# Kernel tuning notes

Measured on AMD Instinct MI355X. Metric: run time of the kernel, lower is better.

The kernel has to match this reference:

```python
import jax, jax.numpy as jnp
import numpy as np

N = 40000            # atoms
ER = 2_500_000       # radial edges
EA = 1_200_000       # angular edges
P = 4_000_000        # angle triples
NUM_SPECIES = 4      # H,C,N,O
CUTOFF = 5.2
ANG_CUTOFF = 3.5
RADIAL_ETA = 16.0
ANGULAR_ETA = 8.0
RDIV = 16
ADIV = 4
ZETA = 32.0
ASEC = 4
RSTART = 0.8
ASTART = 0.8


def setup_inputs() -> dict:
    key = jax.random.key(0)
    ks = jax.random.split(key, 12)
    species = jax.random.randint(ks[0], (N,), 0, NUM_SPECIES, dtype=jnp.int32)
    rad_distances = jax.random.uniform(ks[1], (ER,), jnp.float32, RSTART, CUTOFF)
    rad_switch = jax.random.uniform(ks[2], (ER,), jnp.float32)
    edge_src = jax.random.randint(ks[3], (ER,), 0, N, dtype=jnp.int32)
    edge_dst = jax.random.randint(ks[4], (ER,), 0, N, dtype=jnp.int32)
    ang_distances = jax.random.uniform(ks[5], (EA,), jnp.float32, ASTART, ANG_CUTOFF)
    ang_switch = jax.random.uniform(ks[6], (EA,), jnp.float32)
    angles = jax.random.uniform(ks[7], (P,), jnp.float32, 0.0, float(np.pi))
    central_atom = jax.random.randint(ks[8], (P,), 0, N, dtype=jnp.int32)
    angle_src = jax.random.randint(ks[9], (P,), 0, EA, dtype=jnp.int32)
    angle_dst = jax.random.randint(ks[10], (P,), 0, EA, dtype=jnp.int32)
    ang_edge_dst = jax.random.randint(ks[11], (EA,), 0, N, dtype=jnp.int32)
    return {
        "species": species,
        "rad_distances": rad_distances,
        "rad_switch": rad_switch,
        "edge_src": edge_src,
        "edge_dst": edge_dst,
        "ang_distances": ang_distances,
        "ang_switch": ang_switch,
        "angles": angles,
        "central_atom": central_atom,
        "angle_src": angle_src,
        "angle_dst": angle_dst,
        "ang_edge_dst": ang_edge_dst,
    }


def _triu_table(nsp):
    s1, s2 = np.triu_indices(nsp, 0)
    t = np.zeros((nsp, nsp), dtype=np.int32)
    t[s1, s2] = np.arange(s1.shape[0], dtype=np.int32)
    t[s2, s1] = t[s1, s2]
    return jnp.asarray(t)


def reference(species, rad_distances, rad_switch, edge_src, edge_dst,
              ang_distances, ang_switch, angles, central_atom,
              angle_src, angle_dst, ang_edge_dst):
    n_atoms = species.shape[0]
    nsp = NUM_SPECIES
    nsp_pair = nsp * (nsp + 1) // 2
    indices = species  # already species-order indices in [0, nsp)

    # ---- radial AEV ----
    shiftR = jnp.asarray(-np.linspace(RSTART, CUTOFF, RDIV + 1)[None, :-1],
                         dtype=rad_distances.dtype)  # [1, RDIV]
    x2 = RADIAL_ETA * (rad_distances[:, None] + shiftR) ** 2       # [ER, RDIV]
    radial_terms = jnp.exp(-x2) * (0.25 * rad_switch)[:, None]
    radial_index = edge_src * nsp + indices[edge_dst]
    radial_aev = jax.ops.segment_sum(radial_terms, radial_index,
                                     num_segments=nsp * n_atoms)
    radial_aev = radial_aev.reshape(n_atoms, nsp * RDIV)

    # ---- angular AEV ----
    dist = 0.5 * ANGULAR_ETA ** 0.5 * ang_distances                # [EA]
    d12 = (dist[angle_src] + dist[angle_dst])[:, None]             # [P, 1]
    angle_start = np.pi / (2 * ASEC)
    shiftZ = jnp.asarray(-(np.linspace(0, np.pi, ASEC + 1) + angle_start)[None, :-1],
                         dtype=dist.dtype)                          # [1, ASEC]
    shiftA = jnp.asarray(-ANGULAR_ETA ** 0.5 *
                         np.linspace(ASTART, ANG_CUTOFF, ADIV + 1)[None, :-1],
                         dtype=dist.dtype)                          # [1, ADIV]
    sw = ang_switch * (2.0 * 0.5 ** ZETA) ** 0.5                   # [EA]
    f1 = sw[angle_src] * sw[angle_dst]                             # [P]
    factor1 = f1[:, None] * (1 + jnp.cos(angles[:, None] + shiftZ)) ** ZETA  # [P, ASEC]
    factor2 = jnp.exp(-(d12 + shiftA) ** 2)                        # [P, ADIV]
    angular_terms = (factor1[:, None, :] * factor2[:, :, None]).reshape(-1, ASEC * ADIV)

    idx_dest = indices[ang_edge_dst]                               # [EA]
    triu = _triu_table(nsp)
    angular_index = central_atom * nsp_pair + triu[idx_dest[angle_src], idx_dest[angle_dst]]
    angular_aev = jax.ops.segment_sum(angular_terms, angular_index,
                                      num_segments=nsp_pair * n_atoms)
    angular_aev = angular_aev.reshape(n_atoms, nsp_pair * ASEC * ADIV)

    return jnp.concatenate((radial_aev, angular_aev), axis=-1)     # [N, 224]
```

## Files before the change

### kernel.cpp

```cpp
#include <hip/hip_runtime.h>


constexpr int kOutCols  = 224;
constexpr int kAngBase  = 64;
constexpr int kABUCK    = 64;
constexpr int kMaxBins  = 640;
constexpr int kSCap     = 4096;
constexpr int kNBR      = 640;
constexpr int kNBA      = 1024;
constexpr int kRCap     = 4608;
constexpr int kACap     = 7168;
constexpr int kRC       = 12;
constexpr int kCapR     = 16;
constexpr int kCapA     = 12;
constexpr int kOvf      = 512;

__device__ __constant__ int c_triu[16] = {0,1,2,3, 1,4,5,6, 2,5,7,8, 3,6,8,9};
__device__ __constant__ float c_ca[4] = {0.92387953f, 0.38268343f, -0.38268343f, -0.92387953f};
__device__ __constant__ float c_sa[4] = {0.38268343f, 0.92387953f,  0.92387953f,  0.38268343f};
__device__ __constant__ float c_sh[4] = {-2.2627417f, -4.1719303f, -6.0811183f, -7.9903066f};

constexpr float kThQ  = 20860.437f;
constexpr float kRevD = 7.6295109e-6f;
constexpr float kD12B = 2.2627417f;
constexpr float kD12S = 1.4974026e-2f;
constexpr float kF1D  = 1.1732081e-13f;
constexpr float kRdS  = 930.6818f;
constexpr float kRdD  = 1.0744811e-3f;
constexpr float kRswD = 6.1050061e-5f;

__device__ __forceinline__ int scan1024_exc(int cv, int tid, int* wsum, int* total)
{
    int lane = tid & 63, wv = tid >> 6;
    int x = cv;
    #pragma unroll
    for (int o = 1; o < 64; o <<= 1) {
        int t = __shfl_up(x, o, 64);
        if (lane >= o) x += t;
    }
    if (lane == 63) wsum[wv] = x;
    __syncthreads();
    if (wv == 0 && lane < 16) {
        int s = wsum[lane];
        #pragma unroll
        for (int o = 1; o < 16; o <<= 1) {
            int t = __shfl_up(s, o, 64);
            if (lane >= o) s += t;
        }
        wsum[lane] = s;
    }
    __syncthreads();
    int base = (wv == 0) ? 0 : wsum[wv - 1];
    *total = wsum[15];
    return base + x - cv;
}

__global__ __launch_bounds__(1024)
void fused1(const float* __restrict__ rd, const float* __restrict__ rsw,
            const int* __restrict__ esrc, const int* __restrict__ edst,
            const int* __restrict__ species,
            unsigned* __restrict__ rrec, int* __restrict__ offRT, int ER, int chR,
            const float* __restrict__ ang_d, const float* __restrict__ ang_sw,
            const int* __restrict__ aed, unsigned short* __restrict__ eaq, int EA)
{
    __shared__ unsigned stage[kMaxBins * kCapR];
    __shared__ int cur[kMaxBins], off[kMaxBins + 1];
    __shared__ int wsum[16];
    __shared__ int ovfn;
    __shared__ uint4 ovfb[kOvf];
    int tid = threadIdx.x;

    if (blockIdx.x < kNBR) {
        for (int t = tid; t < kMaxBins; t += 1024) cur[t] = t * kCapR;
        if (tid == 0) ovfn = 0;
        __syncthreads();
        int sb  = blockIdx.x;
        int beg = sb * chR, end = min(beg + chR, ER);
        int i0 = beg + tid * 4;
        if (i0 < end) {
            float4 d4 = *reinterpret_cast<const float4*>(rd + i0);
            float4 s4 = *reinterpret_cast<const float4*>(rsw + i0);
            int4   e4 = *reinterpret_cast<const int4*>(esrc + i0);
            int4   t4 = *reinterpret_cast<const int4*>(edst + i0);
            unsigned sa = (unsigned)species[t4.x], sb2 = (unsigned)species[t4.y];
            unsigned sc2 = (unsigned)species[t4.z], sd = (unsigned)species[t4.w];
            auto bld = [](float d, float s, int e, unsigned sp, unsigned& v, int& k) {
                unsigned qd = min((unsigned)(fmaxf(d - 0.8f, 0.0f) * kRdS + 0.5f), 4095u);
                unsigned qs = min((unsigned)(fmaxf(s, 0.0f) * 4095.0f + 0.5f), 4095u);
                v = qd | (qs << 12) | (sp << 24) | ((unsigned)(e & 63) << 26);
                k = e >> 6;
            };
            unsigned v0, v1, v2, v3; int k0, k1, k2, k3;
            bld(d4.x, s4.x, e4.x, sa,  v0, k0);
            bld(d4.y, s4.y, e4.y, sb2, v1, k1);
            bld(d4.z, s4.z, e4.z, sc2, v2, k2);
            bld(d4.w, s4.w, e4.w, sd,  v3, k3);
            auto ins = [&](int k, unsigned v) {
                int pos = atomicAdd(&cur[k], 1);
                int loc = pos - k * kCapR;
                if (loc < kCapR) stage[pos] = v;
                else {
                    int o = atomicAdd(&ovfn, 1);
                    if (o < kOvf) { ovfb[o].x = (unsigned)k; ovfb[o].y = (unsigned)loc; ovfb[o].z = v; }
                }
            };
            ins(k0, v0); ins(k1, v1); ins(k2, v2); ins(k3, v3);
        }
        __syncthreads();
        int cv = (tid < kMaxBins) ? (cur[tid] - tid * kCapR) : 0;
        int tot;
        int exc = scan1024_exc(cv, tid, wsum, &tot);
        if (tid < kMaxBins) off[tid] = exc;
        if (tid == 0) off[kMaxBins] = tot;
        if (tid < kMaxBins) cur[tid] = min(cv, kCapR);
        __syncthreads();
        for (int s = tid; s < kMaxBins * kCapR; s += 1024) {
            int bin = s >> 4, loc = s & (kCapR - 1);
            if (loc < cur[bin]) rrec[beg + off[bin] + loc] = stage[s];
        }
        int no = min(ovfn, kOvf);
        for (int o = tid; o < no; o += 1024) {
            uint4 e = ovfb[o];
            rrec[beg + off[e.x] + (int)e.y] = e.z;
        }
        for (int t = tid; t <= kMaxBins; t += 1024) offRT[t * kNBR + sb] = off[t];
    } else {
        int i = (blockIdx.x - kNBR) * 1024 + tid;
        if (i < EA) {
            float dq = fmaxf(ang_d[i] - 0.8f, 0.0f) * (255.0f / 2.7f);
            unsigned qd = min((unsigned)(dq + 0.5f), 255u);
            unsigned qs = min((unsigned)(fmaxf(ang_sw[i], 0.0f) * 63.0f + 0.5f), 63u);
            unsigned sp = (unsigned)species[aed[i]];
            eaq[i] = (unsigned short)(qd | (qs << 8) | (sp << 14));
        }
    }
}

__global__ __launch_bounds__(1024)
void fused2(const float* __restrict__ angles, const int* __restrict__ cat,
            const int* __restrict__ asrc, const int* __restrict__ adst,
            const unsigned short* __restrict__ eaq,
            uint2* __restrict__ arec, int* __restrict__ offAT, int P, int chA,
            const unsigned* __restrict__ rrec, const int* __restrict__ offRT,
            int chR, float* __restrict__ out, int N)
{
    __shared__ uint4 raw[4680];
    int tid = threadIdx.x;

    if (blockIdx.x < kNBA) {
        uint2* sbuf = (uint2*)raw;
        int*   cur  = (int*)((char*)raw + 61440);
        int*   off  = (int*)((char*)raw + 64000);
        int*   wsum = (int*)((char*)raw + 66564);
        int*   ovfn = (int*)((char*)raw + 66628);
        uint4* ovfb = (uint4*)((char*)raw + 66640);

        for (int t = tid; t < kMaxBins; t += 1024) cur[t] = t * kCapA;
        if (tid == 0) *ovfn = 0;
        __syncthreads();
        int sb  = blockIdx.x;
        int beg = sb * chA, end = min(beg + chA, P);
        int i0 = beg + tid * 4;
        if (i0 < end) {
            uint4  s4 = *reinterpret_cast<const uint4*>(asrc + i0);
            uint4  d4 = *reinterpret_cast<const uint4*>(adst + i0);
            float4 t4 = *reinterpret_cast<const float4*>(angles + i0);
            int4   c4 = *reinterpret_cast<const int4*>(cat + i0);
            unsigned qa0 = eaq[s4.x], qb0 = eaq[d4.x];
            unsigned qa1 = eaq[s4.y], qb1 = eaq[d4.y];
            unsigned qa2 = eaq[s4.z], qb2 = eaq[d4.z];
            unsigned qa3 = eaq[s4.w], qb3 = eaq[d4.w];
            auto bld = [](unsigned qa, unsigned qb, float th, int atom, uint2& rv, int& key) {
                unsigned qd12 = (qa & 255u) + (qb & 255u);
                unsigned qf1  = ((qa >> 8) & 63u) * ((qb >> 8) & 63u);
                int pair = c_triu[(qa >> 14) * 4 + (qb >> 14)];
                unsigned qt = min((unsigned)(fmaxf(th, 0.0f) * kThQ + 0.5f), 65535u);
                rv.x = qt | (qd12 << 16);
                rv.y = qf1 | ((unsigned)((atom & 63) * 10 + pair) << 16);
                key = atom >> 6;
            };
            uint2 r0, r1, r2, r3; int k0, k1, k2, k3;
            bld(qa0, qb0, t4.x, c4.x, r0, k0);
            bld(qa1, qb1, t4.y, c4.y, r1, k1);
            bld(qa2, qb2, t4.z, c4.z, r2, k2);
            bld(qa3, qb3, t4.w, c4.w, r3, k3);
            auto ins = [&](int k, uint2 r) {
                int pos = atomicAdd(&cur[k], 1);
                int loc = pos - k * kCapA;
                if (loc < kCapA) sbuf[pos] = r;
                else {
                    int o = atomicAdd(ovfn, 1);
                    if (o < kOvf) { ovfb[o].x = (unsigned)k; ovfb[o].y = (unsigned)loc; ovfb[o].z = r.x; ovfb[o].w = r.y; }
                }
            };
            ins(k0, r0); ins(k1, r1); ins(k2, r2); ins(k3, r3);
        }
        __syncthreads();
        int cv = (tid < kMaxBins) ? (cur[tid] - tid * kCapA) : 0;
        int tot;
        int exc = scan1024_exc(cv, tid, wsum, &tot);
        if (tid < kMaxBins) off[tid] = exc;
        if (tid == 0) off[kMaxBins] = tot;
        if (tid < kMaxBins) cur[tid] = min(cv, kCapA);
        __syncthreads();
        for (int s = tid; s < kMaxBins * kCapA; s += 1024) {
            int bin = s / kCapA, loc = s - bin * kCapA;
            if (loc < cur[bin]) arec[beg + off[bin] + loc] = sbuf[s];
        }
        int no = min(*ovfn, kOvf);
        for (int o = tid; o < no; o += 1024) {
            uint4 e = ovfb[o];
            uint2 r; r.x = e.z; r.y = e.w;
            arec[beg + off[e.x] + (int)e.y] = r;
        }
        for (int t = tid; t <= kMaxBins; t += 1024) offAT[t * kNBA + sb] = off[t];
    } else {
        unsigned* rb  = (unsigned*)raw;
        int*      cnt = (int*)((char*)raw + 18432);
        int*      off = (int*)((char*)raw + 18688);
        int*      cur = (int*)((char*)raw + 18948);

        int b = blockIdx.x - kNBA;
        int gstart = 0, glen = 0;
        if (tid < kNBR) {
            int s0 = offRT[b * kNBR + tid];
            int s1 = offRT[(b + 1) * kNBR + tid];
            gstart = tid * chR + s0;
            glen   = s1 - s0;
        }
        unsigned rr[kRC];
        int gl = min(glen, kRC);
        #pragma unroll
        for (int q = 0; q < kRC; ++q) if (q < gl) rr[q] = rrec[gstart + q];
        if (tid < 64) cnt[tid] = 0;
        __syncthreads();
        #pragma unroll
        for (int q = 0; q < kRC; ++q) if (q < gl) atomicAdd(&cnt[(rr[q] >> 26) & 63], 1);
        for (int p = gstart + kRC; p < gstart + glen; ++p)
            atomicAdd(&cnt[(rrec[p] >> 26) & 63], 1);
        __syncthreads();
        if (tid < 64) {
            int x = cnt[tid], v = x;
            #pragma unroll
            for (int o = 1; o < 64; o <<= 1) {
                int t = __shfl_up(v, o, 64);
                if (tid >= o) v += t;
            }
            off[tid] = v - x; cur[tid] = v - x;
            if (tid == 63) off[64] = v;
        }
        __syncthreads();
        #pragma unroll
        for (int q = 0; q < kRC; ++q)
            if (q < gl) {
                int pos = atomicAdd(&cur[(rr[q] >> 26) & 63], 1);
                if (pos < kRCap) rb[pos] = rr[q];
            }
        for (int p = gstart + kRC; p < gstart + glen; ++p) {
            unsigned r = rrec[p];
            int pos = atomicAdd(&cur[(r >> 26) & 63], 1);
            if (pos < kRCap) rb[pos] = r;
        }
        __syncthreads();
        int lane = tid & 63, wave = tid >> 6;
        int q = lane >> 4, k = lane & 15;
        float ck = fmaf(0.275f, (float)k, 0.8f);
        for (int row = wave; row < kABUCK; row += 16) {
            int s  = min(off[row], kRCap);
            int e1 = min(off[row + 1], kRCap);
            float a0 = 0, a1 = 0, a2 = 0, a3 = 0;
            for (int p = s + q; p < e1; p += 4) {
                unsigned r = rb[p];
                float d  = fmaf((float)(r & 4095u), kRdD, 0.8f);
                float sw = (float)((r >> 12) & 4095u) * kRswD;
                int sp   = (r >> 24) & 3;
                float x  = d - ck;
                float v  = sw * __expf(-16.0f * x * x);
                a0 += (sp == 0) ? v : 0.0f;
                a1 += (sp == 1) ? v : 0.0f;
                a2 += (sp == 2) ? v : 0.0f;
                a3 += (sp == 3) ? v : 0.0f;
            }
            a0 += __shfl_xor(a0, 16, 64); a0 += __shfl_xor(a0, 32, 64);
            a1 += __shfl_xor(a1, 16, 64); a1 += __shfl_xor(a1, 32, 64);
            a2 += __shfl_xor(a2, 16, 64); a2 += __shfl_xor(a2, 32, 64);
            a3 += __shfl_xor(a3, 16, 64); a3 += __shfl_xor(a3, 32, 64);
            float val = (q == 0) ? a0 : (q == 1) ? a1 : (q == 2) ? a2 : a3;
            int atom = b * kABUCK + row;
            if (atom < N) out[(size_t)atom * kOutCols + lane] = val;
        }
    }
}

__global__ __launch_bounds__(1024)
void acc_ang(const uint2* __restrict__ arec, const int* __restrict__ offAT,
             int chA, float* __restrict__ out, int N)
{
    __shared__ uint2 ab[kACap];
    __shared__ int cnt[640], off[641], cur[640];
    __shared__ int wsum[16];
    int b = blockIdx.x, tid = threadIdx.x;
    int s0 = offAT[b * kNBA + tid];
    int s1 = offAT[(b + 1) * kNBA + tid];
    int gstart = tid * chA + s0;
    int glen   = s1 - s0;
    uint2 rr[kRC];
    int gl = min(glen, kRC);
    #pragma unroll
    for (int q = 0; q < kRC; ++q) if (q < gl) rr[q] = arec[gstart + q];
    for (int t = tid; t < 640; t += 1024) cnt[t] = 0;
    __syncthreads();
    #pragma unroll
    for (int q = 0; q < kRC; ++q) if (q < gl) atomicAdd(&cnt[rr[q].y >> 16], 1);
    for (int p = gstart + kRC; p < gstart + glen; ++p)
        atomicAdd(&cnt[arec[p].y >> 16], 1);
    __syncthreads();
    int cv = (tid < 640) ? cnt[tid] : 0;
    int tot;
    int exc = scan1024_exc(cv, tid, wsum, &tot);
    if (tid < 640) { off[tid] = exc; cur[tid] = exc; }
    if (tid == 0) off[640] = tot;
    __syncthreads();
    #pragma unroll
    for (int q = 0; q < kRC; ++q)
        if (q < gl) {
            int pos = atomicAdd(&cur[rr[q].y >> 16], 1);
            if (pos < kACap) ab[pos] = rr[q];
        }
    for (int p = gstart + kRC; p < gstart + glen; ++p) {
        uint2 r = arec[p];
        int pos = atomicAdd(&cur[r.y >> 16], 1);
        if (pos < kACap) ab[pos] = r;
    }
    __syncthreads();
    int g = tid >> 4, lam = tid & 15;
    int q = lam >> 2, j = lam & 3;
    float caj = c_ca[j], saj = c_sa[j];
    int atom = b * kABUCK + g;
    if (atom < N) {
        float* orow = out + (size_t)atom * kOutCols + kAngBase;
        for (int pr = 0; pr < 10; ++pr) {
            int s  = min(off[g * 10 + pr], kACap);
            int e1 = min(off[g * 10 + pr + 1], kACap);
            float s0v = 0, s1v = 0, s2v = 0, s3v = 0;
            for (int p = s + q; p < e1; p += 4) {
                uint2 r = ab[p];
                float rev = (float)(r.x & 0xFFFFu) * kRevD;
                float d12 = fmaf((float)(r.x >> 16), kD12S, kD12B);
                float f1  = (float)(r.y & 0xFFFFu) * kF1D;
                float sn, cs;
                asm("v_sin_f32 %0, %1" : "=v"(sn) : "v"(rev));
                asm("v_cos_f32 %0, %1" : "=v"(cs) : "v"(rev));
                float cj = fmaf(cs, caj, sn * saj);
                float t  = 1.0f + cj;
                float t2 = t * t, t4 = t2 * t2, t8 = t4 * t4, t16 = t8 * t8;
                float w  = f1 * (t16 * t16);
                float x0 = d12 + c_sh[0]; s0v = fmaf(w, __expf(-x0 * x0), s0v);
                float x1 = d12 + c_sh[1]; s1v = fmaf(w, __expf(-x1 * x1), s1v);
                float x2 = d12 + c_sh[2]; s2v = fmaf(w, __expf(-x2 * x2), s2v);
                float x3 = d12 + c_sh[3]; s3v = fmaf(w, __expf(-x3 * x3), s3v);
            }
            s0v += __shfl_xor(s0v, 4, 64); s0v += __shfl_xor(s0v, 8, 64);
            s1v += __shfl_xor(s1v, 4, 64); s1v += __shfl_xor(s1v, 8, 64);
            s2v += __shfl_xor(s2v, 4, 64); s2v += __shfl_xor(s2v, 8, 64);
            s3v += __shfl_xor(s3v, 4, 64); s3v += __shfl_xor(s3v, 8, 64);
            float val = (q == 0) ? s0v : (q == 1) ? s1v : (q == 2) ? s2v : s3v;
            orow[pr * 16 + lam] = val;
        }
    }
}

__global__ void radial_kernel(const float* __restrict__ rd, const float* __restrict__ rsw,
                              const int* __restrict__ esrc, const int* __restrict__ edst,
                              const int* __restrict__ species,
                              float* __restrict__ out, int ER)
{
    int i = blockIdx.x * blockDim.x + threadIdx.x;
    if (i >= ER) return;
    float d   = rd[i];
    float sw  = 0.25f * rsw[i];
    int   src = esrc[i];
    int   sp  = species[edst[i]];
    float* base = out + (size_t)src * kOutCols + sp * 16;
    float t = (d - 0.8f) * (1.0f / 0.275f);
    int klo = max(0, (int)ceilf(t - 4.0f));
    int khi = min(15, (int)floorf(t + 4.0f));
    for (int k = klo; k <= khi; ++k) {
        float x = d - fmaf(0.275f, (float)k, 0.8f);
        float v = sw * __expf(-16.0f * x * x);
        if (v > 1e-8f) unsafeAtomicAdd(base + k, v);
    }
}

__global__ void angular_fallback(const float* __restrict__ angles, const int* __restrict__ cat,
                                 const int* __restrict__ asrc, const int* __restrict__ adst,
                                 const float* __restrict__ ang_d, const float* __restrict__ ang_sw,
                                 const int* __restrict__ aed, const int* __restrict__ species,
                                 float* __restrict__ out, int P)
{
    int i = blockIdx.x * blockDim.x + threadIdx.x;
    if (i >= P) return;
    int e1i = asrc[i], e2i = adst[i];
    float d1 = 1.41421356237f * ang_d[e1i];
    float d2 = 1.41421356237f * ang_d[e2i];
    float w1 = 2.1579187e-05f * ang_sw[e1i];
    float w2 = 2.1579187e-05f * ang_sw[e2i];
    int sp1 = species[aed[e1i]], sp2 = species[aed[e2i]];
    float d12 = d1 + d2;
    float f1  = w1 * w2;
    int pair = c_triu[sp1 * 4 + sp2];
    float* base = out + (size_t)cat[i] * kOutCols + kAngBase + pair * 16;

    float s, c;
    __sincosf(angles[i], &s, &c);
    const float ca0 = 0.92387953f, sa0 = 0.38268343f;
    float cth[4];
    cth[0] = fmaf(c,  ca0, s * sa0);
    cth[1] = fmaf(c,  sa0, s * ca0);
    cth[2] = fmaf(c, -sa0, s * ca0);
    cth[3] = fmaf(c, -ca0, s * sa0);
    float fac1[4];
    #pragma unroll
    for (int j = 0; j < 4; ++j) {
        float t  = 1.0f + cth[j];
        float t2 = t * t, t4 = t2 * t2, t8 = t4 * t4, t16 = t8 * t8;
        fac1[j]  = f1 * (t16 * t16);
    }
    const float shiftA[4] = {-2.2627417f, -4.1719303f, -6.0811183f, -7.9903066f};
    #pragma unroll
    for (int ii = 0; ii < 4; ++ii) {
        float x  = d12 + shiftA[ii];
        float f2 = __expf(-x * x);
        if (f2 < 1e-7f) continue;
        #pragma unroll
        for (int j = 0; j < 4; ++j) {
            float v = f2 * fac1[j];
            if (v > 1e-8f) unsafeAtomicAdd(base + ii * 4 + j, v);
        }
    }
}

extern "C" void kernel_launch(void* const* d_in, const int* in_sizes, int n_in,
                              void* d_out, int out_size, void* d_ws, size_t ws_size,
                              hipStream_t stream)
{
    const int*   species = (const int*)  d_in[0];
    const float* rad_d   = (const float*)d_in[1];
    const float* rad_sw  = (const float*)d_in[2];
    const int*   esrc    = (const int*)  d_in[3];
    const int*   edst    = (const int*)  d_in[4];
    const float* ang_d   = (const float*)d_in[5];
    const float* ang_sw  = (const float*)d_in[6];
    const float* angles  = (const float*)d_in[7];
    const int*   cat     = (const int*)  d_in[8];
    const int*   asrc    = (const int*)  d_in[9];
    const int*   adst    = (const int*)  d_in[10];
    const int*   aed     = (const int*)  d_in[11];
    float* out = (float*)d_out;

    const int N  = in_sizes[0];
    const int ER = in_sizes[1];
    const int EA = in_sizes[5];
    const int P  = in_sizes[7];

    const int NB  = (N + kABUCK - 1) / kABUCK;
    const int chR = (((ER + kNBR - 1) / kNBR) + 3) & ~3;
    const int chA = (((P  + kNBA - 1) / kNBA) + 3) & ~3;
    const int prepB = (EA + 1023) / 1024;

    char* w = (char*)d_ws;
    size_t pos = 0;
    auto take = [&](size_t nbytes) {
        size_t cur = pos;
        pos = (pos + nbytes + 255) & ~(size_t)255;
        return cur;
    };
    size_t ea_o   = take((size_t)EA * 2);
    size_t rrec_o = take((size_t)kNBR * chR * 4);
    size_t arec_o = take((size_t)kNBA * chA * 8);
    size_t ort_o  = take((size_t)(kMaxBins + 1) * kNBR * 4);
    size_t oat_o  = take((size_t)(kMaxBins + 1) * kNBA * 4);
    const size_t need = pos;

    const bool sorted_ok = (ws_size >= need) && (NB <= kMaxBins) &&
                           (chR <= kSCap) && (chA <= kSCap) &&
                           ((P & 3) == 0) && ((ER & 3) == 0);

    if (sorted_ok) {
        unsigned short* eaq = (unsigned short*)(w + ea_o);
        unsigned* rrec  = (unsigned*)(w + rrec_o);
        uint2*    arec  = (uint2*)(w + arec_o);
        int*      offRT = (int*)(w + ort_o);
        int*      offAT = (int*)(w + oat_o);

        fused1<<<kNBR + prepB, 1024, 0, stream>>>(rad_d, rad_sw, esrc, edst, species,
                                                  rrec, offRT, ER, chR,
                                                  ang_d, ang_sw, aed, eaq, EA);
        fused2<<<kNBA + NB, 1024, 0, stream>>>(angles, cat, asrc, adst, eaq,
                                               arec, offAT, P, chA,
                                               rrec, offRT, chR, out, N);
        acc_ang<<<NB, 1024, 0, stream>>>(arec, offAT, chA, out, N);
    } else {
        hipMemsetAsync(d_out, 0, (size_t)out_size * sizeof(float), stream);
        radial_kernel<<<(ER + 255) / 256, 256, 0, stream>>>(rad_d, rad_sw, esrc, edst, species, out, ER);
        angular_fallback<<<(P + 255) / 256, 256, 0, stream>>>(angles, cat, asrc, adst,
                                                              ang_d, ang_sw, aed, species, out, P);
    }
}
```

Before: 172.8 us.

## Interleave block roles in fused kernels and batch angular-edge prep per block

```diff
diff --git a/kernel.cpp b/kernel.cpp
--- a/kernel.cpp
+++ b/kernel.cpp
@@ -14,6 +14,7 @@
 constexpr int kCapR     = 16;
 constexpr int kCapA     = 12;
 constexpr int kOvf      = 512;
+constexpr int kPrepE    = 8192;
 
 __device__ __constant__ int c_triu[16] = {0,1,2,3, 1,4,5,6, 2,5,7,8, 3,6,8,9};
 __device__ __constant__ float c_ca[4] = {0.92387953f, 0.38268343f, -0.38268343f, -0.92387953f};
@@ -29,6 +30,15 @@
 constexpr float kRdD  = 1.0744811e-3f;
 constexpr float kRswD = 6.1050061e-5f;
 
+__device__ __forceinline__ bool role_split(int b, int TOT, int NP, int& pidx, int& sidx)
+{
+    long long lo = ((long long)b * NP) / TOT;
+    long long hi = ((long long)(b + 1) * NP) / TOT;
+    pidx = (int)lo;
+    sidx = b - (int)lo;
+    return hi > lo;
+}
+
 __device__ __forceinline__ int scan1024_exc(int cv, int tid, int* wsum, int* total)
 {
     int lane = tid & 63, wv = tid >> 6;
@@ -61,7 +71,8 @@
             const int* __restrict__ species,
             unsigned* __restrict__ rrec, int* __restrict__ offRT, int ER, int chR,
             const float* __restrict__ ang_d, const float* __restrict__ ang_sw,
-            const int* __restrict__ aed, unsigned short* __restrict__ eaq, int EA)
+            const int* __restrict__ aed, unsigned short* __restrict__ eaq, int EA,
+            int TOT)
 {
     __shared__ unsigned stage[kMaxBins * kCapR];
     __shared__ int cur[kMaxBins], off[kMaxBins + 1];
@@ -69,12 +80,13 @@
     __shared__ int ovfn;
     __shared__ uint4 ovfb[kOvf];
     int tid = threadIdx.x;
-
-    if (blockIdx.x < kNBR) {
+    int sb, pid;
+    bool is_scat = role_split(blockIdx.x, TOT, kNBR, sb, pid);
+
+    if (is_scat) {
         for (int t = tid; t < kMaxBins; t += 1024) cur[t] = t * kCapR;
         if (tid == 0) ovfn = 0;
         __syncthreads();
-        int sb  = blockIdx.x;
         int beg = sb * chR, end = min(beg + chR, ER);
         int i0 = beg + tid * 4;
         if (i0 < end) {
@@ -95,8 +107,11 @@
             bld(d4.y, s4.y, e4.y, sb2, v1, k1);
             bld(d4.z, s4.z, e4.z, sc2, v2, k2);
             bld(d4.w, s4.w, e4.w, sd,  v3, k3);
-            auto ins = [&](int k, unsigned v) {
-                int pos = atomicAdd(&cur[k], 1);
+            int pos0 = atomicAdd(&cur[k0], 1);
+            int pos1 = atomicAdd(&cur[k1], 1);
+            int pos2 = atomicAdd(&cur[k2], 1);
+            int pos3 = atomicAdd(&cur[k3], 1);
+            auto put = [&](int pos, int k, unsigned v) {
                 int loc = pos - k * kCapR;
                 if (loc < kCapR) stage[pos] = v;
                 else {
@@ -104,7 +119,7 @@
                     if (o < kOvf) { ovfb[o].x = (unsigned)k; ovfb[o].y = (unsigned)loc; ovfb[o].z = v; }
                 }
             };
-            ins(k0, v0); ins(k1, v1); ins(k2, v2); ins(k3, v3);
+            put(pos0, k0, v0); put(pos1, k1, v1); put(pos2, k2, v2); put(pos3, k3, v3);
         }
         __syncthreads();
         int cv = (tid < kMaxBins) ? (cur[tid] - tid * kCapR) : 0;
@@ -125,13 +140,17 @@
         }
         for (int t = tid; t <= kMaxBins; t += 1024) offRT[t * kNBR + sb] = off[t];
     } else {
-        int i = (blockIdx.x - kNBR) * 1024 + tid;
-        if (i < EA) {
-            float dq = fmaxf(ang_d[i] - 0.8f, 0.0f) * (255.0f / 2.7f);
-            unsigned qd = min((unsigned)(dq + 0.5f), 255u);
-            unsigned qs = min((unsigned)(fmaxf(ang_sw[i], 0.0f) * 63.0f + 0.5f), 63u);
-            unsigned sp = (unsigned)species[aed[i]];
-            eaq[i] = (unsigned short)(qd | (qs << 8) | (sp << 14));
+        int base = pid * kPrepE;
+        #pragma unroll
+        for (int e = 0; e < 8; ++e) {
+            int i = base + e * 1024 + tid;
+            if (i < EA) {
+                float dq = fmaxf(ang_d[i] - 0.8f, 0.0f) * (255.0f / 2.7f);
+                unsigned qd = min((unsigned)(dq + 0.5f), 255u);
+                unsigned qs = min((unsigned)(fmaxf(ang_sw[i], 0.0f) * 63.0f + 0.5f), 63u);
+                unsigned sp = (unsigned)species[aed[i]];
+                eaq[i] = (unsigned short)(qd | (qs << 8) | (sp << 14));
+            }
         }
     }
 }
@@ -142,12 +161,14 @@
             const unsigned short* __restrict__ eaq,
             uint2* __restrict__ arec, int* __restrict__ offAT, int P, int chA,
             const unsigned* __restrict__ rrec, const int* __restrict__ offRT,
-            int chR, float* __restrict__ out, int N)
+            int chR, float* __restrict__ out, int N, int TOT)
 {
     __shared__ uint4 raw[4680];
     int tid = threadIdx.x;
-
-    if (blockIdx.x < kNBA) {
+    int sb, accb;
+    bool is_scat = role_split(blockIdx.x, TOT, kNBA, sb, accb);
+
+    if (is_scat) {
         uint2* sbuf = (uint2*)raw;
         int*   cur  = (int*)((char*)raw + 61440);
         int*   off  = (int*)((char*)raw + 64000);
@@ -158,7 +179,6 @@
         for (int t = tid; t < kMaxBins; t += 1024) cur[t] = t * kCapA;
         if (tid == 0) *ovfn = 0;
         __syncthreads();
-        int sb  = blockIdx.x;
         int beg = sb * chA, end = min(beg + chA, P);
         int i0 = beg + tid * 4;
         if (i0 < end) {
@@ -184,8 +204,11 @@
             bld(qa1, qb1, t4.y, c4.y, r1, k1);
             bld(qa2, qb2, t4.z, c4.z, r2, k2);
             bld(qa3, qb3, t4.w, c4.w, r3, k3);
-            auto ins = [&](int k, uint2 r) {
-                int pos = atomicAdd(&cur[k], 1);
+            int pos0 = atomicAdd(&cur[k0], 1);
+            int pos1 = atomicAdd(&cur[k1], 1);
+            int pos2 = atomicAdd(&cur[k2], 1);
+            int pos3 = atomicAdd(&cur[k3], 1);
+            auto put = [&](int pos, int k, uint2 r) {
                 int loc = pos - k * kCapA;
                 if (loc < kCapA) sbuf[pos] = r;
                 else {
@@ -193,7 +216,7 @@
                     if (o < kOvf) { ovfb[o].x = (unsigned)k; ovfb[o].y = (unsigned)loc; ovfb[o].z = r.x; ovfb[o].w = r.y; }
                 }
             };
-            ins(k0, r0); ins(k1, r1); ins(k2, r2); ins(k3, r3);
+            put(pos0, k0, r0); put(pos1, k1, r1); put(pos2, k2, r2); put(pos3, k3, r3);
         }
         __syncthreads();
         int cv = (tid < kMaxBins) ? (cur[tid] - tid * kCapA) : 0;
@@ -220,7 +243,7 @@
         int*      off = (int*)((char*)raw + 18688);
         int*      cur = (int*)((char*)raw + 18948);
 
-        int b = blockIdx.x - kNBA;
+        int b = accb;
         int gstart = 0, glen = 0;
         if (tid < kNBR) {
             int s0 = offRT[b * kNBR + tid];
@@ -466,7 +489,9 @@
     const int NB  = (N + kABUCK - 1) / kABUCK;
     const int chR = (((ER + kNBR - 1) / kNBR) + 3) & ~3;
     const int chA = (((P  + kNBA - 1) / kNBA) + 3) & ~3;
-    const int prepB = (EA + 1023) / 1024;
+    const int prepB = (EA + kPrepE - 1) / kPrepE;
+    const int TOT1 = kNBR + prepB;
+    const int TOT2 = kNBA + NB;
 
     char* w = (char*)d_ws;
     size_t pos = 0;
@@ -493,12 +518,12 @@
         int*      offRT = (int*)(w + ort_o);
         int*      offAT = (int*)(w + oat_o);
 
-        fused1<<<kNBR + prepB, 1024, 0, stream>>>(rad_d, rad_sw, esrc, edst, species,
-                                                  rrec, offRT, ER, chR,
-                                                  ang_d, ang_sw, aed, eaq, EA);
-        fused2<<<kNBA + NB, 1024, 0, stream>>>(angles, cat, asrc, adst, eaq,
-                                               arec, offAT, P, chA,
-                                               rrec, offRT, chR, out, N);
+        fused1<<<TOT1, 1024, 0, stream>>>(rad_d, rad_sw, esrc, edst, species,
+                                          rrec, offRT, ER, chR,
+                                          ang_d, ang_sw, aed, eaq, EA, TOT1);
+        fused2<<<TOT2, 1024, 0, stream>>>(angles, cat, asrc, adst, eaq,
+                                          arec, offAT, P, chA,
+                                          rrec, offRT, chR, out, N, TOT2);
         acc_ang<<<NB, 1024, 0, stream>>>(arec, offAT, chA, out, N);
     } else {
         hipMemsetAsync(d_out, 0, (size_t)out_size * sizeof(float), stream);
```

After: 179.3 us. 3.8% more time.
